# Kernel optimization log

Measured on AMD Instinct MI355X. Metric: run time of the kernel, lower is better.

## Reference

```python
import jax, jax.numpy as jnp
import numpy as np
import math

B_, M_, T_, E_ = 4, 4, 128, 512
S_ = M_ * T_
H_ = 2048
NE, NS, TOPK, NHEAD = 8, 2, 2, 4
P_, GRUH, AK, AV = 128, 128, 64, 64


def _ln(x, s, b, eps=1e-5):
    mu = x.mean(-1, keepdims=True)
    var = x.var(-1, keepdims=True)
    return (x - mu) / jnp.sqrt(var + eps) * s + b


def _gru(x, Wih, bih, Whh, bhh):
    # x: [N, T, D] -> [N, T, GRUH]; torch nn.GRU cell equations
    Hh = Whh.shape[1]
    def step(h, xt):
        gi = xt @ Wih.T + bih
        gh = h @ Whh.T + bhh
        ir, iz, inn = jnp.split(gi, 3, axis=-1)
        hr, hz, hn = jnp.split(gh, 3, axis=-1)
        r = jax.nn.sigmoid(ir + hr)
        z = jax.nn.sigmoid(iz + hz)
        n = jnp.tanh(inn + r * hn)
        h = (1.0 - z) * n + z * h
        return h, h
    h0 = jnp.zeros((x.shape[0], Hh), x.dtype)
    _, hs = jax.lax.scan(step, h0, jnp.swapaxes(x, 0, 1))
    return jnp.swapaxes(hs, 0, 1)


def _router_logits(x4, rU, rR, rS, Wtp, btp, Wq, bq, Wk, bk, Wv, bv,
                   gWih, gbih, gWhh, gbhh, mW1, mb1, mW2, mb2):
    B, M, T, E = x4.shape
    proc = jax.nn.relu(x4 @ Wtp + btp)                  # [B,M,T,P]
    q = proc @ Wq + bq                                   # [B,M,T,AK]
    Rp = jnp.transpose(rR, (0, 3, 1, 2))                 # [B,T,M,M]
    Sp = jnp.transpose(rS, (0, 3, 1, 2))
    others = np.array([[j for j in range(M) if j != m] for m in range(M)])  # [M,M-1]
    mi = np.arange(M)[:, None]
    feat = jnp.stack([Rp[:, :, mi, others], Sp[:, :, mi, others]], axis=-1)  # [B,T,M,M-1,2]
    keys = feat @ Wk + bk                                # [B,T,M,M-1,AK]
    vals = feat @ Wv + bv                                # [B,T,M,M-1,AV]
    sc = jnp.einsum('bmtk,btmok->bmto', q, keys) / math.sqrt(AK)
    ctx = jnp.einsum('bmto,btmov->bmtv', jax.nn.softmax(sc, -1), vals)  # [B,M,T,AV]
    gin = jnp.concatenate([rU[..., None], ctx], -1).reshape(B * M, T, 1 + AV)
    hs = _gru(gin, gWih, gbih, gWhh, gbhh).reshape(B, M, T, GRUH)
    comb = jnp.concatenate([proc, hs], -1)               # [B,M,T,P+GRUH]
    return jax.nn.relu(comb @ mW1 + mb1) @ mW2 + mb2     # [B,M,T,NE]


def _forward(x, rU, rR, rS, M, T, Wtp, btp, Wq, bq, Wk, bk, Wv, bv,
             gWih, gbih, gWhh, gbhh, mW1, mb1, mW2, mb2,
             sWq, sbq, sWk, sbk, sWv, sbv, sWo, sbo, sln1s, sln1b,
             sW1, sb1, sW2, sb2, sln2s, sln2b, fW1, fb1, fW2, fb2):
    B, S, E = x.shape
    x4 = x.reshape(B, M, T, E)
    logits = _router_logits(x4, rU, rR, rS, Wtp, btp, Wq, bq, Wk, bk, Wv, bv,
                            gWih, gbih, gWhh, gbhh, mW1, mb1, mW2, mb2)
    NT = B * S
    lf = logits.reshape(NT, NE)
    probs = jax.nn.softmax(lf, -1)
    vals, idx = jax.lax.top_k(lf, TOPK)
    tw = jax.nn.softmax(vals, -1)                        # renormalized top-k weights
    tok = x.reshape(NT, E)
    out = jnp.zeros((NT, E), x.dtype)
    hd = E // NHEAD
    for e in range(NE):
        w = jnp.sum(jnp.where(idx == e, tw, 0.0), -1)    # [NT] per-token weight for expert e
        if e < NS:
            # synergy expert: self-attention restricted to tokens routed here.
            # Sort routed tokens to the front (fixed capacity NT) and mask keys.
            valid = w > 0
            order = jnp.argsort(jnp.where(valid, 0, 1), stable=True)
            xg, vg = tok[order], valid[order]
            qh = (xg @ sWq[e] + sbq[e]).reshape(NT, NHEAD, hd)
            kh = (xg @ sWk[e] + sbk[e]).reshape(NT, NHEAD, hd)
            vh = (xg @ sWv[e] + sbv[e]).reshape(NT, NHEAD, hd)
            sc = jnp.einsum('nhd,mhd->hnm', qh, kh) / math.sqrt(hd)
            sc = jnp.where(vg[None, None, :], sc, -1e9)
            ao = jnp.einsum('hnm,mhd->nhd', jax.nn.softmax(sc, -1), vh).reshape(NT, E)
            ao = ao @ sWo[e] + sbo[e]
            h1 = _ln(xg + ao, sln1s[e], sln1b[e])
            ff = jax.nn.relu(h1 @ sW1[e] + sb1[e]) @ sW2[e] + sb2[e]
            y = _ln(h1 + ff, sln2s[e], sln2b[e])
            out = out.at[order].add(y * w[order][:, None])
        else:
            # FFN expert is pointwise -> dense compute weighted by w (w==0 elsewhere)
            f = e - NS
            y = jax.nn.relu(tok @ fW1[f] + fb1[f]) @ fW2[f] + fb2[f]
            out = out + y * w[:, None]
    return (out.reshape(B, S, E), probs.reshape(B, M, T, NE),
            idx.reshape(B, M, T, TOPK))


def setup_inputs() -> dict:
    key = jax.random.key(0)
    ks = iter(jax.random.split(key, 64))
    def rn(shape, s=0.02):
        return jax.random.normal(next(ks), shape, dtype=jnp.float32) * s
    Cm = (P_ + GRUH) // 2
    return {
        'x': jax.random.normal(next(ks), (B_, S_, E_), dtype=jnp.float32),
        'rU': jax.random.uniform(next(ks), (B_, M_, T_), dtype=jnp.float32),
        'rR': jax.random.uniform(next(ks), (B_, M_, M_, T_), dtype=jnp.float32),
        'rS': jax.random.uniform(next(ks), (B_, M_, M_, T_), dtype=jnp.float32),
        'M': M_, 'T': T_,
        'Wtp': rn((E_, P_)), 'btp': jnp.zeros((P_,)),
        'Wq': rn((P_, AK)), 'bq': jnp.zeros((AK,)),
        'Wk': rn((2, AK)), 'bk': jnp.zeros((AK,)),
        'Wv': rn((2, AV)), 'bv': jnp.zeros((AV,)),
        'gWih': rn((3 * GRUH, 1 + AV)), 'gbih': jnp.zeros((3 * GRUH,)),
        'gWhh': rn((3 * GRUH, GRUH)), 'gbhh': jnp.zeros((3 * GRUH,)),
        'mW1': rn((P_ + GRUH, Cm)), 'mb1': jnp.zeros((Cm,)),
        'mW2': rn((Cm, NE)), 'mb2': jnp.zeros((NE,)),
        'sWq': rn((NS, E_, E_)), 'sbq': jnp.zeros((NS, E_)),
        'sWk': rn((NS, E_, E_)), 'sbk': jnp.zeros((NS, E_)),
        'sWv': rn((NS, E_, E_)), 'sbv': jnp.zeros((NS, E_)),
        'sWo': rn((NS, E_, E_)), 'sbo': jnp.zeros((NS, E_)),
        'sln1s': jnp.ones((NS, E_)), 'sln1b': jnp.zeros((NS, E_)),
        'sW1': rn((NS, E_, H_)), 'sb1': jnp.zeros((NS, H_)),
        'sW2': rn((NS, H_, E_)), 'sb2': jnp.zeros((NS, E_)),
        'sln2s': jnp.ones((NS, E_)), 'sln2b': jnp.zeros((NS, E_)),
        'fW1': rn((NE - NS, E_, H_)), 'fb1': jnp.zeros((NE - NS, H_)),
        'fW2': rn((NE - NS, H_, E_)), 'fb2': jnp.zeros((NE - NS, E_)),
    }


def reference(x, rU, rR, rS, M, T, Wtp, btp, Wq, bq, Wk, bk, Wv, bv,
              gWih, gbih, gWhh, gbhh, mW1, mb1, mW2, mb2,
              sWq, sbq, sWk, sbk, sWv, sbv, sWo, sbo, sln1s, sln1b,
              sW1, sb1, sW2, sb2, sln2s, sln2b, fW1, fb1, fW2, fb2):
    return _forward(x, rU, rR, rS, M, T, Wtp, btp, Wq, bq, Wk, bk, Wv, bv,
                    gWih, gbih, gWhh, gbhh, mW1, mb1, mW2, mb2,
                    sWq, sbq, sWk, sbk, sWv, sbv, sWo, sbo, sln1s, sln1b,
                    sW1, sb1, sW2, sb2, sln2s, sln2b, fW1, fb1, fW2, fb2)
```

## Files before the change

kernel.cpp:

```cpp
#include <hip/hip_runtime.h>
#include <math.h>

#define Bc 4
#define Mc 4
#define Tc 128
#define Ec 512
#define Hc 2048
#define NEc 8
#define NSc 2
#define NHEADc 4
#define Pc 128
#define GRUHc 128
#define AKc 64
#define AVc 64
#define NTc 2048
#define HDc 128

typedef __bf16 bfv8 __attribute__((ext_vector_type(8)));
typedef float f32x4 __attribute__((ext_vector_type(4)));
typedef float f32v16 __attribute__((ext_vector_type(16)));

__global__ __launch_bounds__(256)
void zero_k(float* __restrict__ out, int* __restrict__ cnt)
{
    int i = blockIdx.x * 256 + threadIdx.x;
    float4* o4 = (float4*)out;
    if (i < (NTc * Ec) / 4) o4[i] = make_float4(0.f, 0.f, 0.f, 0.f);
    if (i < NEc) cnt[i] = 0;
}

struct CJob { const float* src; __bf16* dst; };
struct CJobs8 { CJob j[8]; };

__global__ __launch_bounds__(256)
void convT_k(CJobs8 jobs, int K, int N)
{
    CJob J = jobs.j[blockIdx.z];
    __shared__ float t[32][33];
    int bx = blockIdx.x * 32;
    int by = blockIdx.y * 32;
    int tx = threadIdx.x & 31, ty = threadIdx.x >> 5;
#pragma unroll
    for (int i = 0; i < 4; ++i) {
        int k = by + ty + i * 8, n = bx + tx;
        t[ty + i * 8][tx] = (k < K && n < N) ? J.src[(size_t)k * N + n] : 0.f;
    }
    __syncthreads();
#pragma unroll
    for (int i = 0; i < 4; ++i) {
        int n = bx + ty + i * 8, k = by + tx;
        if (n < N && k < K) J.dst[(size_t)n * K + k] = (__bf16)t[tx][ty + i * 8];
    }
}

__global__ __launch_bounds__(256)
void gemm_k(const float* __restrict__ A, int lda,
            const float* __restrict__ B, int ldb,
            const float* __restrict__ bias,
            float* __restrict__ C, int ldc,
            int M, int N, int K, int relu)
{
    int tm = blockIdx.x * 64, tn = blockIdx.y * 64;
    if (tm >= M || tn >= N) return;
    __shared__ float As[16][68];
    __shared__ float Bs[16][68];
    int tid = threadIdx.x;
    int tx = tid & 15, ty = tid >> 4;
    float acc[4][4] = {};
    int arow = tid >> 2;
    int ak0  = (tid & 3) * 4;
    int bk   = tid >> 4;
    int bc0  = (tid & 15) * 4;
    int grA = tm + arow;
    const float* Arow = (grA < M) ? (A + (size_t)grA * lda) : nullptr;

    for (int k0 = 0; k0 < K; k0 += 16) {
#pragma unroll
        for (int u = 0; u < 4; ++u) {
            int k = k0 + ak0 + u;
            As[ak0 + u][arow] = (Arow && k < K) ? Arow[k] : 0.f;
        }
        int kb = k0 + bk;
#pragma unroll
        for (int u = 0; u < 4; ++u) {
            int n2 = tn + bc0 + u;
            Bs[bk][bc0 + u] = (kb < K && n2 < N) ? B[(size_t)kb * ldb + n2] : 0.f;
        }
        __syncthreads();
#pragma unroll
        for (int kk = 0; kk < 16; ++kk) {
            float a0 = As[kk][ty * 4 + 0], a1 = As[kk][ty * 4 + 1];
            float a2 = As[kk][ty * 4 + 2], a3 = As[kk][ty * 4 + 3];
            float b0 = Bs[kk][tx * 4 + 0], b1 = Bs[kk][tx * 4 + 1];
            float b2 = Bs[kk][tx * 4 + 2], b3 = Bs[kk][tx * 4 + 3];
            acc[0][0] += a0 * b0; acc[0][1] += a0 * b1; acc[0][2] += a0 * b2; acc[0][3] += a0 * b3;
            acc[1][0] += a1 * b0; acc[1][1] += a1 * b1; acc[1][2] += a1 * b2; acc[1][3] += a1 * b3;
            acc[2][0] += a2 * b0; acc[2][1] += a2 * b1; acc[2][2] += a2 * b2; acc[2][3] += a2 * b3;
            acc[3][0] += a3 * b0; acc[3][1] += a3 * b1; acc[3][2] += a3 * b2; acc[3][3] += a3 * b3;
        }
        __syncthreads();
    }
#pragma unroll
    for (int i = 0; i < 4; ++i) {
        int gr = tm + ty * 4 + i;
        if (gr >= M) continue;
#pragma unroll
        for (int j = 0; j < 4; ++j) {
            int gc = tn + tx * 4 + j;
            if (gc >= N) continue;
            float v = acc[i][j] + (bias ? bias[gc] : 0.f);
            if (relu) v = fmaxf(v, 0.f);
            C[(size_t)gr * ldc + gc] = v;
        }
    }
}

struct GJob {
    const void* A;
    const void* B;
    const float* bias;
    void* C;
    const int* Mptr;
    const int* gatherA;
    float* scatterOut;
    const int* scatterList;
    const float* wvec;
    int ldc;
    int flags;
};
struct GJobs6 { GJob j[6]; };

#define LDA_S 40
template<int AMODE>
__global__ __launch_bounds__(256)
void gemm_batch_k(GJobs6 jobs, int lda, int ldb, int N, int K,
                  int nTilesY, int kIters)
{
    GJob J = jobs.j[blockIdx.z];
    int M = *J.Mptr;
    int by = blockIdx.y;
    int ny = by % nTilesY, ko = by / nTilesY;
    int tm = blockIdx.x * 128, tn = ny * 128;
    if (tm >= M || tn >= N) return;
    int KT = K / 32;
    int kt0 = ko * kIters;
    int ktE = kt0 + kIters; if (ktE > KT) ktE = KT;
    if (kt0 >= KT) return;

    __shared__ __bf16 As[128 * LDA_S];
    __shared__ __bf16 Bs[128 * LDA_S];
    int tid = threadIdx.x, lane = tid & 63, wvi = tid >> 6;
    int wm = (wvi & 1) * 64, wn = (wvi >> 1) * 64;
    f32x4 acc[4][4] = {};

    int ar = tid >> 1, ah = (tid & 1) * 16;
    const float*  Apf = nullptr;
    const __bf16* Apb = nullptr;
    if (tm + ar < M) {
        int g = J.gatherA ? J.gatherA[tm + ar] : (tm + ar);
        if (AMODE == 0) Apf = (const float*)J.A + (size_t)g * lda;
        else            Apb = (const __bf16*)J.A + (size_t)g * lda;
    }
    const __bf16* Bp = ((tn + ar) < N) ? ((const __bf16*)J.B + (size_t)(tn + ar) * ldb)
                                       : nullptr;

    float fa[16];
    bfv8 ra0, ra1, rb0, rb1;

    auto LOADA = [&](int k0) {
        int kb = k0 + ah;
        if (AMODE == 0) {
            if (Apf) {
                const float4* p = (const float4*)(Apf + kb);
                float4 x0 = p[0], x1 = p[1], x2 = p[2], x3 = p[3];
                fa[0]=x0.x; fa[1]=x0.y; fa[2]=x0.z; fa[3]=x0.w;
                fa[4]=x1.x; fa[5]=x1.y; fa[6]=x1.z; fa[7]=x1.w;
                fa[8]=x2.x; fa[9]=x2.y; fa[10]=x2.z; fa[11]=x2.w;
                fa[12]=x3.x; fa[13]=x3.y; fa[14]=x3.z; fa[15]=x3.w;
            } else {
#pragma unroll
                for (int i = 0; i < 16; ++i) fa[i] = 0.f;
            }
        } else {
            if (Apb) {
                ra0 = *(const bfv8*)(Apb + kb);
                ra1 = *(const bfv8*)(Apb + kb + 8);
            } else {
#pragma unroll
                for (int i = 0; i < 8; ++i) { ra0[i] = (__bf16)0.f; ra1[i] = (__bf16)0.f; }
            }
        }
    };
    auto LOADB = [&](int k0) {
        int kb = k0 + ah;
        if (Bp) {
            rb0 = *(const bfv8*)(Bp + kb);
            rb1 = *(const bfv8*)(Bp + kb + 8);
        } else {
#pragma unroll
            for (int i = 0; i < 8; ++i) { rb0[i] = (__bf16)0.f; rb1[i] = (__bf16)0.f; }
        }
    };

    LOADA(kt0 * 32);
    LOADB(kt0 * 32);

    for (int kt = kt0; kt < ktE; ++kt) {
        __syncthreads();
        if (AMODE == 0) {
            bfv8 p0, p1;
#pragma unroll
            for (int i = 0; i < 8; ++i) { p0[i] = (__bf16)fa[i]; p1[i] = (__bf16)fa[8 + i]; }
            *(bfv8*)(As + ar * LDA_S + ah) = p0;
            *(bfv8*)(As + ar * LDA_S + ah + 8) = p1;
        } else {
            *(bfv8*)(As + ar * LDA_S + ah) = ra0;
            *(bfv8*)(As + ar * LDA_S + ah + 8) = ra1;
        }
        *(bfv8*)(Bs + ar * LDA_S + ah) = rb0;
        *(bfv8*)(Bs + ar * LDA_S + ah + 8) = rb1;
        __syncthreads();
        if (kt + 1 < ktE) {
            LOADA((kt + 1) * 32);
            LOADB((kt + 1) * 32);
        }
        {
            int fr = lane & 15, quad = lane >> 4;
            bfv8 af[4], bfr[4];
            const __bf16* Ab = As + quad * 8 + fr * LDA_S;
            const __bf16* Bb2 = Bs + quad * 8 + fr * LDA_S;
#pragma unroll
            for (int t2 = 0; t2 < 4; ++t2) {
                af[t2]  = *(const bfv8*)(Ab + (wm + t2 * 16) * LDA_S);
                bfr[t2] = *(const bfv8*)(Bb2 + (wn + t2 * 16) * LDA_S);
            }
#pragma unroll
            for (int i = 0; i < 4; ++i)
#pragma unroll
                for (int j = 0; j < 4; ++j)
                    acc[i][j] = __builtin_amdgcn_mfma_f32_16x16x32_bf16(af[i], bfr[j], acc[i][j], 0, 0, 0);
        }
    }

    int col = lane & 15, rq = (lane >> 4) * 4;
    int relu = J.flags & 1, storeT = J.flags & 2, storeBf = J.flags & 4;
    int addBias = (J.bias != nullptr) && (ko == 0);
#pragma unroll
    for (int ti = 0; ti < 4; ++ti) {
#pragma unroll
        for (int tj = 0; tj < 4; ++tj) {
#pragma unroll
            for (int r = 0; r < 4; ++r) {
                int gm = tm + wm + ti * 16 + rq + r;
                int gn = tn + wn + tj * 16 + col;
                if (gm < M && gn < N) {
                    float v = acc[ti][tj][r] + (addBias ? J.bias[gn] : 0.f);
                    if (relu) v = fmaxf(v, 0.f);
                    if (J.scatterOut) {
                        int g = J.scatterList[gm];
                        atomicAdd(&J.scatterOut[(size_t)g * Ec + gn], v * J.wvec[(size_t)g * NEc]);
                    } else if (storeT) {
                        ((float*)J.C)[(size_t)gn * J.ldc + gm] = v;
                    } else if (storeBf) {
                        ((__bf16*)J.C)[(size_t)gm * J.ldc + gn] = (__bf16)v;
                    } else {
                        ((float*)J.C)[(size_t)gm * J.ldc + gn] = v;
                    }
                }
            }
        }
    }
}

__global__ __launch_bounds__(256)
void flash_k(const float* __restrict__ QbB, const float* __restrict__ KbB,
             const float* __restrict__ VtB, float* __restrict__ AOB,
             const int* __restrict__ cntB)
{
    int e = blockIdx.z;
    const float* Qb = QbB + (size_t)e * NTc * Ec;
    const float* Kb = KbB + (size_t)e * NTc * Ec;
    const float* Vt = VtB + (size_t)e * NTc * Ec;
    float* AO = AOB + (size_t)e * NTc * Ec;
    int nv = cntB[e];
    int r0 = blockIdx.x * 64;
    if (r0 >= nv) return;
    int h = blockIdx.y;
    const int QS = 136, VS = 72;
    __shared__ __bf16 Ql[64 * 136];
    __shared__ __bf16 Kl[64 * 136];
    __shared__ __bf16 Vl[128 * 72];
    __shared__ __bf16 Pl[64 * 72];
    int tid = threadIdx.x, lane = tid & 63, wv = tid >> 6;
    int fr = lane & 15, quad = lane >> 4;

    {
        int qr = tid >> 2, c0 = (tid & 3) * 32;
        const float* src = Qb + (size_t)(r0 + qr) * Ec + h * HDc + c0;
        __bf16* dst = Ql + qr * QS + c0;
        bool ok = (r0 + qr) < nv;
#pragma unroll
        for (int u = 0; u < 8; ++u) {
            float4 v = ok ? ((const float4*)src)[u] : make_float4(0.f, 0.f, 0.f, 0.f);
            dst[u*4+0] = (__bf16)v.x; dst[u*4+1] = (__bf16)v.y;
            dst[u*4+2] = (__bf16)v.z; dst[u*4+3] = (__bf16)v.w;
        }
    }

    f32x4 accO[8];
#pragma unroll
    for (int j = 0; j < 8; ++j) accO[j] = (f32x4){0.f, 0.f, 0.f, 0.f};
    float mrow[4] = {-1e30f, -1e30f, -1e30f, -1e30f};
    float lrow[4] = {0.f, 0.f, 0.f, 0.f};
    const float invsq = 0.08838834764831845f;

    for (int j0 = 0; j0 < nv; j0 += 64) {
        __syncthreads();
        {
            int kr = tid >> 2, c0 = (tid & 3) * 32;
            const float* src = Kb + (size_t)(j0 + kr) * Ec + h * HDc + c0;
            __bf16* dst = Kl + kr * QS + c0;
            bool ok = (j0 + kr) < nv;
#pragma unroll
            for (int u = 0; u < 8; ++u) {
                float4 v = ok ? ((const float4*)src)[u] : make_float4(0.f, 0.f, 0.f, 0.f);
                dst[u*4+0] = (__bf16)v.x; dst[u*4+1] = (__bf16)v.y;
                dst[u*4+2] = (__bf16)v.z; dst[u*4+3] = (__bf16)v.w;
            }
        }
        {
            int dr = tid >> 1, c0 = (tid & 1) * 32;
            const float* src = Vt + (size_t)(h * HDc + dr) * NTc + j0 + c0;
            __bf16* dst = Vl + dr * VS + c0;
            int rem = nv - (j0 + c0);
            if (rem >= 32) {
#pragma unroll
                for (int u = 0; u < 8; ++u) {
                    float4 v = ((const float4*)src)[u];
                    dst[u*4+0] = (__bf16)v.x; dst[u*4+1] = (__bf16)v.y;
                    dst[u*4+2] = (__bf16)v.z; dst[u*4+3] = (__bf16)v.w;
                }
            } else {
                for (int u = 0; u < 32; ++u)
                    dst[u] = (u < rem) ? (__bf16)src[u] : (__bf16)0.f;
            }
        }
        __syncthreads();

        f32x4 sc[4] = {};
#pragma unroll
        for (int ks = 0; ks < 4; ++ks) {
            bfv8 aq = *(const bfv8*)(Ql + (wv * 16 + fr) * QS + ks * 32 + quad * 8);
#pragma unroll
            for (int tj = 0; tj < 4; ++tj) {
                bfv8 bk8 = *(const bfv8*)(Kl + (tj * 16 + fr) * QS + ks * 32 + quad * 8);
                sc[tj] = __builtin_amdgcn_mfma_f32_16x16x32_bf16(aq, bk8, sc[tj], 0, 0, 0);
            }
        }

        float alpha[4];
#pragma unroll
        for (int r = 0; r < 4; ++r) {
            float sv[4];
            float mx = -1e30f;
#pragma unroll
            for (int tj = 0; tj < 4; ++tj) {
                float s = sc[tj][r] * invsq;
                bool valid = (j0 + tj * 16 + fr) < nv;
                s = valid ? s : -1e30f;
                sv[tj] = s;
                mx = fmaxf(mx, s);
            }
#pragma unroll
            for (int off = 1; off < 16; off <<= 1)
                mx = fmaxf(mx, __shfl_xor(mx, off, 64));
            float mn = fmaxf(mrow[r], mx);
            alpha[r] = expf(mrow[r] - mn);
            float ps = 0.f;
#pragma unroll
            for (int tj = 0; tj < 4; ++tj) {
                bool valid = (j0 + tj * 16 + fr) < nv;
                float p = valid ? expf(sv[tj] - mn) : 0.f;
                Pl[(wv * 16 + quad * 4 + r) * VS + tj * 16 + fr] = (__bf16)p;
                ps += p;
            }
#pragma unroll
            for (int off = 1; off < 16; off <<= 1)
                ps += __shfl_xor(ps, off, 64);
            lrow[r] = lrow[r] * alpha[r] + ps;
            mrow[r] = mn;
        }
#pragma unroll
        for (int tj = 0; tj < 8; ++tj)
#pragma unroll
            for (int r = 0; r < 4; ++r)
                accO[tj][r] *= alpha[r];
#pragma unroll
        for (int ks = 0; ks < 2; ++ks) {
            bfv8 ap = *(const bfv8*)(Pl + (wv * 16 + fr) * VS + ks * 32 + quad * 8);
#pragma unroll
            for (int tj = 0; tj < 8; ++tj) {
                bfv8 bv8 = *(const bfv8*)(Vl + (tj * 16 + fr) * VS + ks * 32 + quad * 8);
                accO[tj] = __builtin_amdgcn_mfma_f32_16x16x32_bf16(ap, bv8, accO[tj], 0, 0, 0);
            }
        }
    }

#pragma unroll
    for (int r = 0; r < 4; ++r) {
        int row = r0 + wv * 16 + quad * 4 + r;
        if (row < nv) {
            float invl = 1.f / lrow[r];
#pragma unroll
            for (int tj = 0; tj < 8; ++tj)
                AO[(size_t)row * Ec + h * HDc + tj * 16 + fr] = accO[tj][r] * invl;
        }
    }
}

__global__ __launch_bounds__(256)
void router_ctx_k(const float* __restrict__ q4, const float* __restrict__ rR,
                  const float* __restrict__ rS,
                  const float* __restrict__ Wk, const float* __restrict__ bk,
                  const float* __restrict__ Wv, const float* __restrict__ bv,
                  float* __restrict__ ctx)
{
    int tid = threadIdx.x;
    int lane = tid & 63;
    int n = blockIdx.x * 4 + (tid >> 6);
    int m = (n >> 7) & 3, t = n & 127, b = n >> 9;
    float q = q4[(size_t)n * AKc + lane];
    float sc[3], rv[3], sv[3];
#pragma unroll
    for (int o = 0; o < 3; ++o) {
        int oth = o + (o >= m ? 1 : 0);
        float r = rR[(((size_t)(b * Mc + m)) * Mc + oth) * Tc + t];
        float s_ = rS[(((size_t)(b * Mc + m)) * Mc + oth) * Tc + t];
        rv[o] = r; sv[o] = s_;
        float key = r * Wk[lane] + s_ * Wk[64 + lane] + bk[lane];
        float p = q * key;
#pragma unroll
        for (int off = 32; off; off >>= 1) p += __shfl_xor(p, off, 64);
        sc[o] = p * 0.125f;
    }
    float mx = fmaxf(sc[0], fmaxf(sc[1], sc[2]));
    float e0 = expf(sc[0] - mx), e1 = expf(sc[1] - mx), e2 = expf(sc[2] - mx);
    float inv = 1.f / (e0 + e1 + e2);
    float p0 = e0 * inv, p1 = e1 * inv, p2 = e2 * inv;
    float v0 = rv[0] * Wv[lane] + sv[0] * Wv[64 + lane] + bv[lane];
    float v1 = rv[1] * Wv[lane] + sv[1] * Wv[64 + lane] + bv[lane];
    float v2 = rv[2] * Wv[lane] + sv[2] * Wv[64 + lane] + bv[lane];
    ctx[(size_t)n * AVc + lane] = p0 * v0 + p1 * v1 + p2 * v2;
}

__global__ __launch_bounds__(256)
void gi_k(const float* __restrict__ rU, const float* __restrict__ ctx,
          const float* __restrict__ gWih, const float* __restrict__ gbih,
          float* __restrict__ gi)
{
    int idx = blockIdx.x * 256 + threadIdx.x;
    int g = idx % 384, nt = idx / 384;
    const float* Wr = gWih + (size_t)g * 65;
    float a = gbih[g] + rU[nt] * Wr[0];
    const float* c = ctx + (size_t)nt * AVc;
#pragma unroll
    for (int d = 0; d < 64; ++d) a += c[d] * Wr[1 + d];
    gi[(size_t)nt * 384 + g] = a;
}

__global__ __launch_bounds__(384) __attribute__((amdgpu_waves_per_eu(2, 2)))
void gru_scan_k(const float* __restrict__ gi, const float* __restrict__ gWhh,
                const float* __restrict__ gbhh, float* __restrict__ hs)
{
    int seq = blockIdx.x, g = threadIdx.x;
    __shared__ float h[128];
    __shared__ float gh[384];
    const f32v16* wp = (const f32v16*)(gWhh + (size_t)g * 128);
    f32v16 w0 = wp[0], w1 = wp[1], w2 = wp[2], w3 = wp[3];
    f32v16 w4 = wp[4], w5 = wp[5], w6 = wp[6], w7 = wp[7];
    asm volatile("" : "+v"(w0), "+v"(w1), "+v"(w2), "+v"(w3),
                      "+v"(w4), "+v"(w5), "+v"(w6), "+v"(w7));
    float bh = gbhh[g];
    if (g < 128) h[g] = 0.f;
    float g0 = 0.f, g1 = 0.f, g2 = 0.f;
    if (g < 128) {
        const float* gr = gi + (size_t)seq * 128 * 384;
        g0 = gr[g]; g1 = gr[128 + g]; g2 = gr[256 + g];
    }
    __syncthreads();
    for (int t = 0; t < 128; ++t) {
        float a0 = 0.f, a1 = 0.f, a2 = 0.f, a3 = 0.f;
#define GRU_STEP16(W, B) { \
        float4 x0 = *(const float4*)&h[B];      float4 x1 = *(const float4*)&h[(B) + 4]; \
        float4 x2 = *(const float4*)&h[(B) + 8]; float4 x3 = *(const float4*)&h[(B) + 12]; \
        a0 += x0.x * W[0];  a1 += x0.y * W[1];  a2 += x0.z * W[2];  a3 += x0.w * W[3]; \
        a0 += x1.x * W[4];  a1 += x1.y * W[5];  a2 += x1.z * W[6];  a3 += x1.w * W[7]; \
        a0 += x2.x * W[8];  a1 += x2.y * W[9];  a2 += x2.z * W[10]; a3 += x2.w * W[11]; \
        a0 += x3.x * W[12]; a1 += x3.y * W[13]; a2 += x3.z * W[14]; a3 += x3.w * W[15]; }
        GRU_STEP16(w0, 0)   GRU_STEP16(w1, 16)  GRU_STEP16(w2, 32)  GRU_STEP16(w3, 48)
        GRU_STEP16(w4, 64)  GRU_STEP16(w5, 80)  GRU_STEP16(w6, 96)  GRU_STEP16(w7, 112)
#undef GRU_STEP16
        gh[g] = bh + (a0 + a1) + (a2 + a3);
        __syncthreads();
        if (g < 128) {
            float r = 1.f / (1.f + expf(-(g0 + gh[g])));
            float z = 1.f / (1.f + expf(-(g1 + gh[128 + g])));
            float nn = tanhf(g2 + r * gh[256 + g]);
            float hn = (1.f - z) * nn + z * h[g];
            hs[((size_t)seq * 128 + t) * 128 + g] = hn;
            h[g] = hn;
            if (t + 1 < 128) {
                const float* gr = gi + ((size_t)seq * 128 + t + 1) * 384;
                g0 = gr[g]; g1 = gr[128 + g]; g2 = gr[256 + g];
            }
        }
        __syncthreads();
    }
}

__global__ __launch_bounds__(128)
void mlp_route_k(const float* __restrict__ proc, const float* __restrict__ hs,
                 const float* __restrict__ mW1, const float* __restrict__ mb1,
                 const float* __restrict__ mW2, const float* __restrict__ mb2,
                 float* __restrict__ probsOut, float* __restrict__ idxOut,
                 float* __restrict__ w)
{
    int n = blockIdx.x, tid = threadIdx.x;
    __shared__ float comb[256], tmp[128], lg[8];
    comb[tid] = proc[(size_t)n * 128 + tid];
    comb[128 + tid] = hs[(size_t)n * 128 + tid];
    __syncthreads();
    float a = mb1[tid];
#pragma unroll 8
    for (int d = 0; d < 256; ++d) a += comb[d] * mW1[(size_t)d * 128 + tid];
    tmp[tid] = fmaxf(a, 0.f);
    __syncthreads();
    if (tid < 8) {
        float l = mb2[tid];
        for (int d = 0; d < 128; ++d) l += tmp[d] * mW2[(size_t)d * 8 + tid];
        lg[tid] = l;
    }
    __syncthreads();
    if (tid == 0) {
        float mx = lg[0];
        for (int e = 1; e < 8; ++e) mx = fmaxf(mx, lg[e]);
        float p[8], s = 0.f;
        for (int e = 0; e < 8; ++e) { p[e] = expf(lg[e] - mx); s += p[e]; }
        float inv = 1.f / s;
        for (int e = 0; e < 8; ++e) probsOut[(size_t)n * 8 + e] = p[e] * inv;
        int a0 = 0; float v0 = lg[0];
        for (int e = 1; e < 8; ++e) if (lg[e] > v0) { v0 = lg[e]; a0 = e; }
        int a1 = -1; float v1 = -1e30f;
        for (int e = 0; e < 8; ++e) if (e != a0 && lg[e] > v1) { v1 = lg[e]; a1 = e; }
        float e1 = expf(v1 - v0);
        float t0 = 1.f / (1.f + e1), t1 = e1 / (1.f + e1);
        idxOut[(size_t)n * 2 + 0] = (float)a0;
        idxOut[(size_t)n * 2 + 1] = (float)a1;
        for (int e = 0; e < 8; ++e) w[(size_t)n * 8 + e] = 0.f;
        w[(size_t)n * 8 + a0] = t0;
        w[(size_t)n * 8 + a1] = t1;
    }
}

__global__ __launch_bounds__(256)
void compact_k(const float* __restrict__ w, int* __restrict__ cnt,
               int* __restrict__ list)
{
    int n = blockIdx.x * 256 + threadIdx.x;
    if (n >= NTc) return;
    for (int e = 0; e < NEc; ++e)
        if (w[(size_t)n * 8 + e] > 0.f) {
            int p = atomicAdd(&cnt[e], 1);
            list[e * NTc + p] = n;
        }
}

__global__ __launch_bounds__(256)
void ln1_k(const float* __restrict__ x, const int* __restrict__ listB,
           const float* __restrict__ addB, const float* __restrict__ sB,
           const float* __restrict__ bB, float* __restrict__ outB,
           const int* __restrict__ cntB)
{
    int e = blockIdx.y;
    int i = blockIdx.x;
    if (i >= cntB[e]) return;
    const int* list = listB + e * NTc;
    const float* add = addB + (size_t)e * NTc * Ec;
    const float* s = sB + e * Ec;
    const float* b = bB + e * Ec;
    float* outRows = outB + (size_t)e * NTc * Ec;
    int tid = threadIdx.x;
    int g = list[i];
    float v0 = x[(size_t)g * Ec + tid] + add[(size_t)i * Ec + tid];
    float v1 = x[(size_t)g * Ec + 256 + tid] + add[(size_t)i * Ec + 256 + tid];
    __shared__ float red[256];
    __shared__ float bc;
    red[tid] = v0 + v1; __syncthreads();
    for (int st = 128; st > 0; st >>= 1) { if (tid < st) red[tid] += red[tid + st]; __syncthreads(); }
    if (tid == 0) bc = red[0] * (1.f / 512.f);
    __syncthreads();
    float mu = bc;
    float d0 = v0 - mu, d1 = v1 - mu;
    __syncthreads();
    red[tid] = d0 * d0 + d1 * d1; __syncthreads();
    for (int st = 128; st > 0; st >>= 1) { if (tid < st) red[tid] += red[tid + st]; __syncthreads(); }
    if (tid == 0) bc = rsqrtf(red[0] * (1.f / 512.f) + 1e-5f);
    __syncthreads();
    float inv = bc;
    outRows[(size_t)i * Ec + tid] = d0 * inv * s[tid] + b[tid];
    outRows[(size_t)i * Ec + 256 + tid] = d1 * inv * s[256 + tid] + b[256 + tid];
}

__global__ __launch_bounds__(256)
void ln2_scatter_k(const float* __restrict__ H1B, const float* __restrict__ YB,
                   const float* __restrict__ sB, const float* __restrict__ bB,
                   float* __restrict__ out, const int* __restrict__ listB,
                   const int* __restrict__ cntB, const float* __restrict__ wB)
{
    int e = blockIdx.y;
    int i = blockIdx.x;
    if (i >= cntB[e]) return;
    const int* list = listB + e * NTc;
    const float* H1 = H1B + (size_t)e * NTc * Ec;
    const float* Y = YB + (size_t)e * NTc * Ec;
    const float* s = sB + e * Ec;
    const float* b = bB + e * Ec;
    const float* wvec = wB + e;
    int tid = threadIdx.x;
    int g = list[i];
    float v0 = H1[(size_t)i * Ec + tid] + Y[(size_t)i * Ec + tid];
    float v1 = H1[(size_t)i * Ec + 256 + tid] + Y[(size_t)i * Ec + 256 + tid];
    __shared__ float red[256];
    __shared__ float bc;
    red[tid] = v0 + v1; __syncthreads();
    for (int st = 128; st > 0; st >>= 1) { if (tid < st) red[tid] += red[tid + st]; __syncthreads(); }
    if (tid == 0) bc = red[0] * (1.f / 512.f);
    __syncthreads();
    float mu = bc;
    float d0 = v0 - mu, d1 = v1 - mu;
    __syncthreads();
    red[tid] = d0 * d0 + d1 * d1; __syncthreads();
    for (int st = 128; st > 0; st >>= 1) { if (tid < st) red[tid] += red[tid + st]; __syncthreads(); }
    if (tid == 0) bc = rsqrtf(red[0] * (1.f / 512.f) + 1e-5f);
    __syncthreads();
    float inv = bc;
    float wv = wvec[(size_t)g * 8];
    atomicAdd(&out[(size_t)g * Ec + tid], (d0 * inv * s[tid] + b[tid]) * wv);
    atomicAdd(&out[(size_t)g * Ec + 256 + tid], (d1 * inv * s[256 + tid] + b[256 + tid]) * wv);
}

extern "C" void kernel_launch(void* const* d_in, const int* in_sizes, int n_in,
                              void* d_out, int out_size, void* d_ws, size_t ws_size,
                              hipStream_t stream)
{
    const float* x    = (const float*)d_in[0];
    const float* rU   = (const float*)d_in[1];
    const float* rR   = (const float*)d_in[2];
    const float* rS   = (const float*)d_in[3];
    const float* Wtp  = (const float*)d_in[6];
    const float* btp  = (const float*)d_in[7];
    const float* Wq   = (const float*)d_in[8];
    const float* bq   = (const float*)d_in[9];
    const float* Wk   = (const float*)d_in[10];
    const float* bk   = (const float*)d_in[11];
    const float* Wv   = (const float*)d_in[12];
    const float* bv   = (const float*)d_in[13];
    const float* gWih = (const float*)d_in[14];
    const float* gbih = (const float*)d_in[15];
    const float* gWhh = (const float*)d_in[16];
    const float* gbhh = (const float*)d_in[17];
    const float* mW1  = (const float*)d_in[18];
    const float* mb1  = (const float*)d_in[19];
    const float* mW2  = (const float*)d_in[20];
    const float* mb2  = (const float*)d_in[21];
    const float* sWq  = (const float*)d_in[22];
    const float* sbq  = (const float*)d_in[23];
    const float* sWk  = (const float*)d_in[24];
    const float* sbk  = (const float*)d_in[25];
    const float* sWv  = (const float*)d_in[26];
    const float* sbv  = (const float*)d_in[27];
    const float* sWo  = (const float*)d_in[28];
    const float* sbo  = (const float*)d_in[29];
    const float* sln1s = (const float*)d_in[30];
    const float* sln1b = (const float*)d_in[31];
    const float* sW1  = (const float*)d_in[32];
    const float* sb1  = (const float*)d_in[33];
    const float* sW2  = (const float*)d_in[34];
    const float* sb2  = (const float*)d_in[35];
    const float* sln2s = (const float*)d_in[36];
    const float* sln2b = (const float*)d_in[37];
    const float* fW1  = (const float*)d_in[38];
    const float* fb1  = (const float*)d_in[39];
    const float* fW2  = (const float*)d_in[40];
    const float* fb2  = (const float*)d_in[41];

    float* out      = (float*)d_out;
    float* probsOut = out + (size_t)NTc * Ec;
    float* idxOut   = probsOut + (size_t)NTc * NEc;

    int*   cnt  = (int*)d_ws;
    int*   list = cnt + 64;
    float* w    = (float*)d_ws + 64 + NEc * NTc;
    __bf16* WB = (__bf16*)(w + NTc * NEc);
    auto QKVO_T = [&](int e, int i) { return WB + ((size_t)(e * 4 + i)) * 262144; };
    __bf16* sW1T = WB + 8 * 262144;
    __bf16* sW2T = sW1T + 2 * 1048576;
    __bf16* fW1T = sW2T + 2 * 1048576;
    __bf16* fW2T = fW1T + 3 * 1048576;
    float* act = (float*)(fW2T + 3 * 1048576);
    float* QbB = act;
    float* KbB = act + 2 * 1048576;
    float* VtB = act + 4 * 1048576;
    float* AOB = act + 6 * 1048576;
    float* H1B = act + 8 * 1048576;
    float* PRJB = QbB;
    float* YbB  = KbB;
    __bf16* FF1syn = (__bf16*)VtB;
    __bf16* FF1ffn = (__bf16*)act;
    __bf16* fW1T2 = FF1ffn + (size_t)3 * NTc * Hc;
    __bf16* fW2T2 = fW1T2 + 3 * 1048576;
    float* proc = act;
    float* q4   = act + 262144;
    float* ctx  = act + 393216;
    float* gi   = act + 524288;
    float* hs   = act + 1310720;

    zero_k<<<1024, 256, 0, stream>>>(out, cnt);

    gemm_k<<<dim3(32, 2), 256, 0, stream>>>(x, Ec, Wtp, Pc, btp, proc, Pc, NTc, Pc, Ec, 1);
    gemm_k<<<dim3(32, 1), 256, 0, stream>>>(proc, Pc, Wq, AKc, bq, q4, AKc, NTc, AKc, Pc, 0);
    router_ctx_k<<<512, 256, 0, stream>>>(q4, rR, rS, Wk, bk, Wv, bv, ctx);
    gi_k<<<3072, 256, 0, stream>>>(rU, ctx, gWih, gbih, gi);
    gru_scan_k<<<16, 384, 0, stream>>>(gi, gWhh, gbhh, hs);
    mlp_route_k<<<2048, 128, 0, stream>>>(proc, hs, mW1, mb1, mW2, mb2,
                                          probsOut, idxOut, w);
    compact_k<<<8, 256, 0, stream>>>(w, cnt, list);

    GJob JZ = {};

    {
        CJobs8 cq = {};
        for (int e = 0; e < 2; ++e) {
            cq.j[e * 4 + 0] = { sWq + (size_t)e * Ec * Ec, QKVO_T(e, 0) };
            cq.j[e * 4 + 1] = { sWk + (size_t)e * Ec * Ec, QKVO_T(e, 1) };
            cq.j[e * 4 + 2] = { sWv + (size_t)e * Ec * Ec, QKVO_T(e, 2) };
            cq.j[e * 4 + 3] = { sWo + (size_t)e * Ec * Ec, QKVO_T(e, 3) };
        }
        convT_k<<<dim3(16, 16, 8), 256, 0, stream>>>(cq, Ec, Ec);
        CJobs8 c1 = {};
        c1.j[0] = { sW1, sW1T };
        c1.j[1] = { sW1 + (size_t)Ec * Hc, sW1T + 1048576 };
        convT_k<<<dim3(64, 16, 2), 256, 0, stream>>>(c1, Ec, Hc);
        CJobs8 c2 = {};
        c2.j[0] = { sW2, sW2T };
        c2.j[1] = { sW2 + (size_t)Hc * Ec, sW2T + 1048576 };
        convT_k<<<dim3(16, 64, 2), 256, 0, stream>>>(c2, Hc, Ec);
    }

    {
        GJobs6 js = {};
        for (int e = 0; e < 2; ++e) {
            GJob jq = JZ;
            jq.A = x; jq.Mptr = cnt + e; jq.gatherA = list + e * NTc;
            jq.B = QKVO_T(e, 0); jq.bias = sbq + e * Ec;
            jq.C = QbB + (size_t)e * NTc * Ec; jq.ldc = Ec; jq.flags = 0;
            GJob jk = jq; jk.B = QKVO_T(e, 1); jk.bias = sbk + e * Ec;
            jk.C = KbB + (size_t)e * NTc * Ec;
            GJob jv = jq; jv.B = QKVO_T(e, 2); jv.bias = sbv + e * Ec;
            jv.C = VtB + (size_t)e * NTc * Ec; jv.ldc = NTc; jv.flags = 2;
            js.j[e * 3 + 0] = jq; js.j[e * 3 + 1] = jk; js.j[e * 3 + 2] = jv;
        }
        gemm_batch_k<0><<<dim3(16, 4, 6), 256, 0, stream>>>(js, Ec, Ec, Ec, Ec, 4, 16);
    }

    flash_k<<<dim3(32, 4, 2), 256, 0, stream>>>(QbB, KbB, VtB, AOB, cnt);

    {
        GJobs6 js = {};
        for (int e = 0; e < 2; ++e) {
            GJob jo = JZ;
            jo.A = AOB + (size_t)e * NTc * Ec; jo.Mptr = cnt + e;
            jo.B = QKVO_T(e, 3); jo.bias = sbo + e * Ec;
            jo.C = PRJB + (size_t)e * NTc * Ec; jo.ldc = Ec;
            js.j[e] = jo;
        }
        gemm_batch_k<0><<<dim3(16, 4, 2), 256, 0, stream>>>(js, Ec, Ec, Ec, Ec, 4, 16);
    }

    ln1_k<<<dim3(2048, 2), 256, 0, stream>>>(x, list, PRJB, sln1s, sln1b, H1B, cnt);

    {
        GJobs6 js = {};
        for (int e = 0; e < 2; ++e) {
            GJob j1 = JZ;
            j1.A = H1B + (size_t)e * NTc * Ec; j1.Mptr = cnt + e;
            j1.B = sW1T + (size_t)e * 1048576; j1.bias = sb1 + (size_t)e * Hc;
            j1.C = FF1syn + (size_t)e * NTc * Hc; j1.ldc = Hc; j1.flags = 1 | 4;
            js.j[e] = j1;
        }
        gemm_batch_k<0><<<dim3(16, 16, 2), 256, 0, stream>>>(js, Ec, Ec, Hc, Ec, 16, 16);
    }

    {
        GJobs6 js = {};
        for (int e = 0; e < 2; ++e) {
            GJob j2 = JZ;
            j2.A = FF1syn + (size_t)e * NTc * Hc; j2.Mptr = cnt + e;
            j2.B = sW2T + (size_t)e * 1048576; j2.bias = sb2 + (size_t)e * Ec;
            j2.C = YbB + (size_t)e * NTc * Ec; j2.ldc = Ec;
            js.j[e] = j2;
        }
        gemm_batch_k<1><<<dim3(16, 4, 2), 256, 0, stream>>>(js, Hc, Hc, Ec, Hc, 4, 64);
    }

    ln2_scatter_k<<<dim3(2048, 2), 256, 0, stream>>>(H1B, YbB, sln2s, sln2b,
                                                     out, list, cnt, w);

    {
        CJobs8 a = {};
        for (int u = 0; u < 6; ++u)
            a.j[u] = { fW1 + (size_t)u * Ec * Hc,
                       (u < 3 ? fW1T + (size_t)u * 1048576
                              : fW1T2 + (size_t)(u - 3) * 1048576) };
        convT_k<<<dim3(64, 16, 6), 256, 0, stream>>>(a, Ec, Hc);
        CJobs8 b = {};
        for (int u = 0; u < 6; ++u)
            b.j[u] = { fW2 + (size_t)u * Hc * Ec,
                       (u < 3 ? fW2T + (size_t)u * 1048576
                              : fW2T2 + (size_t)(u - 3) * 1048576) };
        convT_k<<<dim3(16, 64, 6), 256, 0, stream>>>(b, Hc, Ec);
    }

    for (int rnd = 0; rnd < 2; ++rnd) {
        int f0 = rnd * 3;
        __bf16* W1 = rnd == 0 ? fW1T : fW1T2;
        __bf16* W2 = rnd == 0 ? fW2T : fW2T2;
        {
            GJobs6 js = {};
            for (int u = 0; u < 3; ++u) {
                int f = f0 + u, e = f + NSc;
                GJob j1 = JZ;
                j1.A = x; j1.Mptr = cnt + e; j1.gatherA = list + e * NTc;
                j1.B = W1 + (size_t)u * 1048576; j1.bias = fb1 + (size_t)f * Hc;
                j1.C = FF1ffn + (size_t)u * NTc * Hc; j1.ldc = Hc; j1.flags = 1 | 4;
                js.j[u] = j1;
            }
            gemm_batch_k<0><<<dim3(16, 16, 3), 256, 0, stream>>>(js, Ec, Ec, Hc, Ec, 16, 16);
        }
        {
            GJobs6 js = {};
            for (int u = 0; u < 3; ++u) {
                int f = f0 + u, e = f + NSc;
                GJob j2 = JZ;
                j2.A = FF1ffn + (size_t)u * NTc * Hc; j2.Mptr = cnt + e;
                j2.B = W2 + (size_t)u * 1048576; j2.bias = fb2 + (size_t)f * Ec;
                j2.scatterOut = out; j2.scatterList = list + e * NTc;
                j2.wvec = w + e; j2.ldc = Ec;
                js.j[u] = j2;
            }
            gemm_batch_k<1><<<dim3(16, 16, 3), 256, 0, stream>>>(js, Hc, Hc, Ec, Hc, 4, 16);
        }
    }
}
```

Baseline: 974.7 us.

## Split GRU recurrent dot products across thread pairs and prefetch gate inputs

The GRU scan kernel now uses 768 threads: each gate row's 128-wide recurrent dot product is split across two lanes that each hold 64 weights in registers, and the halves are combined with a lane shuffle. This halves the serial FMA chain per step on the latency-bound 16-block scan. The next step's input-gate values are loaded at the start of each iteration so the load overlaps the matvec, and the hidden state is kept in a register. Plain __syncthreads is replaced by a raw s_barrier that only waits on LDS counters. The cost is more waves per barrier and an extra shuffle per step.

```diff
diff --git a/kernel.cpp b/kernel.cpp
--- a/kernel.cpp
+++ b/kernel.cpp
@@ -468,53 +468,68 @@
     gi[(size_t)nt * 384 + g] = a;
 }
 
-__global__ __launch_bounds__(384) __attribute__((amdgpu_waves_per_eu(2, 2)))
+__device__ __forceinline__ void wgbar()
+{
+    __builtin_amdgcn_sched_barrier(0);
+    asm volatile("s_waitcnt lgkmcnt(0)" ::: "memory");
+    __builtin_amdgcn_s_barrier();
+    __builtin_amdgcn_sched_barrier(0);
+}
+
+__global__ __launch_bounds__(768)
 void gru_scan_k(const float* __restrict__ gi, const float* __restrict__ gWhh,
                 const float* __restrict__ gbhh, float* __restrict__ hs)
 {
-    int seq = blockIdx.x, g = threadIdx.x;
+    int seq = blockIdx.x, tid = threadIdx.x;
+    int g = tid >> 1, half = tid & 1;
     __shared__ float h[128];
     __shared__ float gh[384];
-    const f32v16* wp = (const f32v16*)(gWhh + (size_t)g * 128);
+    const f32v16* wp = (const f32v16*)(gWhh + (size_t)g * 128 + half * 64);
     f32v16 w0 = wp[0], w1 = wp[1], w2 = wp[2], w3 = wp[3];
-    f32v16 w4 = wp[4], w5 = wp[5], w6 = wp[6], w7 = wp[7];
-    asm volatile("" : "+v"(w0), "+v"(w1), "+v"(w2), "+v"(w3),
-                      "+v"(w4), "+v"(w5), "+v"(w6), "+v"(w7));
+    asm volatile("" : "+v"(w0), "+v"(w1), "+v"(w2), "+v"(w3));
     float bh = gbhh[g];
-    if (g < 128) h[g] = 0.f;
-    float g0 = 0.f, g1 = 0.f, g2 = 0.f;
-    if (g < 128) {
+
+    float hreg = 0.f, c0 = 0.f, c1 = 0.f, c2 = 0.f;
+    if (tid < 128) {
+        h[tid] = 0.f;
         const float* gr = gi + (size_t)seq * 128 * 384;
-        g0 = gr[g]; g1 = gr[128 + g]; g2 = gr[256 + g];
-    }
-    __syncthreads();
+        c0 = gr[tid]; c1 = gr[128 + tid]; c2 = gr[256 + tid];
+    }
+    wgbar();
+
     for (int t = 0; t < 128; ++t) {
+        float n0 = 0.f, n1 = 0.f, n2 = 0.f;
+        if (tid < 128 && t + 1 < 128) {
+            const float* gr = gi + ((size_t)seq * 128 + t + 1) * 384;
+            n0 = gr[tid]; n1 = gr[128 + tid]; n2 = gr[256 + tid];
+        }
         float a0 = 0.f, a1 = 0.f, a2 = 0.f, a3 = 0.f;
+        const float* hb = h + half * 64;
 #define GRU_STEP16(W, B) { \
-        float4 x0 = *(const float4*)&h[B];      float4 x1 = *(const float4*)&h[(B) + 4]; \
-        float4 x2 = *(const float4*)&h[(B) + 8]; float4 x3 = *(const float4*)&h[(B) + 12]; \
+        float4 x0 = *(const float4*)&hb[B];       float4 x1 = *(const float4*)&hb[(B) + 4]; \
+        float4 x2 = *(const float4*)&hb[(B) + 8]; float4 x3 = *(const float4*)&hb[(B) + 12]; \
         a0 += x0.x * W[0];  a1 += x0.y * W[1];  a2 += x0.z * W[2];  a3 += x0.w * W[3]; \
         a0 += x1.x * W[4];  a1 += x1.y * W[5];  a2 += x1.z * W[6];  a3 += x1.w * W[7]; \
         a0 += x2.x * W[8];  a1 += x2.y * W[9];  a2 += x2.z * W[10]; a3 += x2.w * W[11]; \
         a0 += x3.x * W[12]; a1 += x3.y * W[13]; a2 += x3.z * W[14]; a3 += x3.w * W[15]; }
-        GRU_STEP16(w0, 0)   GRU_STEP16(w1, 16)  GRU_STEP16(w2, 32)  GRU_STEP16(w3, 48)
-        GRU_STEP16(w4, 64)  GRU_STEP16(w5, 80)  GRU_STEP16(w6, 96)  GRU_STEP16(w7, 112)
+        GRU_STEP16(w0, 0)  GRU_STEP16(w1, 16)  GRU_STEP16(w2, 32)  GRU_STEP16(w3, 48)
 #undef GRU_STEP16
-        gh[g] = bh + (a0 + a1) + (a2 + a3);
-        __syncthreads();
-        if (g < 128) {
-            float r = 1.f / (1.f + expf(-(g0 + gh[g])));
-            float z = 1.f / (1.f + expf(-(g1 + gh[128 + g])));
-            float nn = tanhf(g2 + r * gh[256 + g]);
-            float hn = (1.f - z) * nn + z * h[g];
-            hs[((size_t)seq * 128 + t) * 128 + g] = hn;
-            h[g] = hn;
-            if (t + 1 < 128) {
-                const float* gr = gi + ((size_t)seq * 128 + t + 1) * 384;
-                g0 = gr[g]; g1 = gr[128 + g]; g2 = gr[256 + g];
-            }
-        }
-        __syncthreads();
+        float s = (a0 + a1) + (a2 + a3);
+        s += __shfl_xor(s, 1, 64);
+        if (half == 0) gh[g] = s + bh;
+        wgbar();
+        if (tid < 128) {
+            float ghr = gh[tid], ghz = gh[128 + tid], ghn = gh[256 + tid];
+            float r  = 1.f / (1.f + expf(-(c0 + ghr)));
+            float z  = 1.f / (1.f + expf(-(c1 + ghz)));
+            float nn = tanhf(c2 + r * ghn);
+            float hn = (1.f - z) * nn + z * hreg;
+            hs[((size_t)seq * 128 + t) * 128 + tid] = hn;
+            h[tid] = hn;
+            hreg = hn;
+            c0 = n0; c1 = n1; c2 = n2;
+        }
+        wgbar();
     }
 }
 
@@ -731,7 +746,7 @@
     gemm_k<<<dim3(32, 1), 256, 0, stream>>>(proc, Pc, Wq, AKc, bq, q4, AKc, NTc, AKc, Pc, 0);
     router_ctx_k<<<512, 256, 0, stream>>>(q4, rR, rS, Wk, bk, Wv, bv, ctx);
     gi_k<<<3072, 256, 0, stream>>>(rU, ctx, gWih, gbih, gi);
-    gru_scan_k<<<16, 384, 0, stream>>>(gi, gWhh, gbhh, hs);
+    gru_scan_k<<<16, 768, 0, stream>>>(gi, gWhh, gbhh, hs);
     mlp_route_k<<<2048, 128, 0, stream>>>(proc, hs, mW1, mb1, mW2, mb2,
                                           probsOut, idxOut, w);
     compact_k<<<8, 256, 0, stream>>>(w, cnt, list);
```

New measurement: 990.7 us. Within noise of the previous version (+1.6%).
